# Kernel tuning notes

Measured on AMD Instinct MI355X. Metric: run time of the kernel, lower is better.

## Reference

```python
import jax, jax.numpy as jnp
import numpy as np

K = 2            # kernel_size
NQ = K * K       # 4 qubits
DEPTH = 1


def _apply1(state, U, q):
    # state: (N,2,2,2,2) complex; apply 2x2 gate U on qubit q
    s = jnp.moveaxis(state, 1 + q, -1)
    s = s @ U.T
    return jnp.moveaxis(s, -1, 1 + q)


def _cnot(state, c, t):
    s = jnp.moveaxis(state, (1 + c, 1 + t), (-2, -1))  # (...,2c,2t)
    s = jnp.stack([s[..., 0, :], s[..., 1, ::-1]], axis=-2)
    return jnp.moveaxis(s, (-2, -1), (1 + c, 1 + t))


def _rx(w):
    c, s = jnp.cos(w / 2), jnp.sin(w / 2)
    return jnp.array([[1, 0], [0, 1]], jnp.complex64) * c + jnp.array([[0, -1j], [-1j, 0]], jnp.complex64) * s


def _ry(w):
    c, s = jnp.cos(w / 2), jnp.sin(w / 2)
    return jnp.array([[1, 0], [0, 1]], jnp.complex64) * c + jnp.array([[0, -1], [1, 0]], jnp.complex64) * s


def setup_inputs() -> dict:
    key = jax.random.key(0)
    k1, k2, k3 = jax.random.split(key, 3)
    B, C, H = 1024, 1, 28
    F = H - K + 1
    n_feat = NQ * C * F * F  # 2916
    x = jax.random.uniform(k1, (B, C, H, H), dtype=jnp.float32)
    W = jax.random.normal(k2, (10, n_feat), dtype=jnp.float32)
    b = jax.random.normal(k3, (10,), dtype=jnp.float32)
    weights = jnp.zeros((DEPTH, NQ), dtype=jnp.float32)  # forward() uses zeros, not the Parameter
    return {"x": x, "W": W, "b": b, "weights": weights}


def reference(x, W, b, weights):
    B, C, H, _ = x.shape
    F = H - K + 1
    # extract all KxK patches, row-major within the patch (matches img[c,i:i+k,j:j+k].reshape(-1))
    p = jnp.stack([x[:, :, i:i + F, j:j + F] for i in range(K) for j in range(K)], axis=-1)  # (B,C,F,F,4)
    ang = p.reshape(-1, NQ) * jnp.pi  # AngleEmbedding angles, (N,4)
    # product state from per-qubit RY(theta)|0> = [cos(t/2), sin(t/2)]
    a = jnp.stack([jnp.cos(ang / 2), jnp.sin(ang / 2)], axis=-1).astype(jnp.complex64)  # (N,4,2)
    state = jnp.einsum('na,nb,nc,nd->nabcd', a[:, 0], a[:, 1], a[:, 2], a[:, 3])
    for l in range(DEPTH):
        w = weights[l]
        state = _apply1(state, _rx(w[0]), 0)
        state = _apply1(state, _rx(w[1]), 1)
        state = _cnot(state, 2, 3)
        state = _cnot(state, 0, 2)
        state = _cnot(state, 0, 3)
        state = _apply1(state, _ry(w[2]), 0)
        state = _apply1(state, _ry(w[3]), 3)
    probs = state.real ** 2 + state.imag ** 2  # (N,2,2,2,2)
    z = jnp.array([1.0, -1.0], dtype=x.dtype)
    evs = []
    for q in range(NQ):
        axes = tuple(ax for ax in range(1, 5) if ax != 1 + q)
        evs.append(probs.sum(axes) @ z)  # <Z_q>, (N,)
    evs = jnp.stack(evs, axis=-1)  # (N, 4)
    # per-image reorder: (C*F*F, 4) -> transpose -> (4*C, F, F)
    q = evs.reshape(B, C, F, F, NQ)
    q = jnp.transpose(q, (0, 4, 1, 2, 3)).reshape(B, NQ * C * F * F)
    return q @ W.T + b
```

## Files before the change

### kernel.cpp

```cpp
#include <hip/hip_runtime.h>


#define HD 28
#define NPIX 784
#define FD 27
#define NPATCH 729
#define NF 2916
#define NG 729
#define NOUT 10
#define PSTR 257
#define IM 2

__global__ __launch_bounds__(256)
void hqnn_fused(const float* __restrict__ x,
                const float* __restrict__ W,
                const float* __restrict__ bias,
                const float* __restrict__ wts,
                float* __restrict__ out)
{
    __shared__ __align__(16) float evl[IM][NF];
    __shared__ union U {
        struct { float sc[IM][NPIX]; float ss[IM][NPIX]; } tr;
        float part[IM * NOUT][PSTR];
    } u;

    const int tid = threadIdx.x;

    const float w0 = wts[0], w1 = wts[1], w2 = wts[2], w3 = wts[3];
    const float cw0 = cosf(w0);
    const float cw1 = cosf(w1);
    const float cw2 = cosf(w2), sw2 = sinf(w2);
    const float cw3 = cosf(w3), sw3 = sinf(w3);

    const float4* xb4 = (const float4*)(x + blockIdx.x * (IM * NPIX));
    for (int t = tid; t < IM * NPIX / 4; t += 256) {
        const float4 v = xb4[t];
        const int p4  = t * 4;
        const int img = (p4 >= NPIX) ? 1 : 0;
        const int off = p4 - img * NPIX;
        float s0, c0, s1, c1, s2, c2, s3, c3;
        sincospif(v.x, &s0, &c0);
        sincospif(v.y, &s1, &c1);
        sincospif(v.z, &s2, &c2);
        sincospif(v.w, &s3, &c3);
        u.tr.sc[img][off]     = c0; u.tr.ss[img][off]     = s0;
        u.tr.sc[img][off + 1] = c1; u.tr.ss[img][off + 1] = s1;
        u.tr.sc[img][off + 2] = c2; u.tr.ss[img][off + 2] = s2;
        u.tr.sc[img][off + 3] = c3; u.tr.ss[img][off + 3] = s3;
    }
    __syncthreads();

    for (int pp = tid; pp < IM * NPATCH; pp += 256) {
        const int img = pp / NPATCH;
        const int pa  = pp - img * NPATCH;
        const int fi  = pa / FD;
        const int fj  = pa - fi * FD;
        const int p   = fi * HD + fj;

        const float c00 = u.tr.sc[img][p];
        const float c01 = u.tr.sc[img][p + 1];
        const float c10 = u.tr.sc[img][p + HD];
        const float c11 = u.tr.sc[img][p + HD + 1];
        const float s00 = u.tr.ss[img][p];
        const float s10 = u.tr.ss[img][p + HD];
        const float s11 = u.tr.ss[img][p + HD + 1];

        const float ev2 = cw0 * c00 * c10;
        evl[img][pa]               = cw2 * cw0 * c00 - sw2 * s00 * s10;
        evl[img][NPATCH + pa]      = cw1 * c01;
        evl[img][2 * NPATCH + pa]  = ev2;
        evl[img][3 * NPATCH + pa]  = cw3 * ev2 * c11 - sw3 * s11;
    }
    __syncthreads();

    float acc[IM][NOUT];
#pragma unroll
    for (int m = 0; m < IM; ++m)
#pragma unroll
        for (int o = 0; o < NOUT; ++o) acc[m][o] = 0.f;

    const float4* W4 = (const float4*)W;
    const float4* e0 = (const float4*)evl[0];
    const float4* e1 = (const float4*)evl[1];
    for (int g = tid; g < NG; g += 256) {
        const float4 a = e0[g];
        const float4 c = e1[g];
#pragma unroll
        for (int o = 0; o < NOUT; ++o) {
            const float4 w = W4[o * NG + g];
            acc[0][o] += a.x * w.x + a.y * w.y + a.z * w.z + a.w * w.w;
            acc[1][o] += c.x * w.x + c.y * w.y + c.z * w.z + c.w * w.w;
        }
    }

#pragma unroll
    for (int m = 0; m < IM; ++m)
#pragma unroll
        for (int o = 0; o < NOUT; ++o) u.part[m * NOUT + o][tid] = acc[m][o];
    __syncthreads();

    if (tid < IM * NOUT * 8) {
        const int row = tid >> 3;
        const int j   = tid & 7;
        float s = 0.f;
#pragma unroll
        for (int k = 0; k < 256; k += 8) s += u.part[row][j + k];
        s += __shfl_down(s, 4, 8);
        s += __shfl_down(s, 2, 8);
        s += __shfl_down(s, 1, 8);
        if (j == 0) {
            const int img = (row >= NOUT) ? 1 : 0;
            const int o   = row - img * NOUT;
            out[(blockIdx.x * IM + img) * NOUT + o] = s + bias[o];
        }
    }
}

extern "C" void kernel_launch(void* const* d_in, const int* in_sizes, int n_in,
                              void* d_out, int out_size, void* d_ws, size_t ws_size,
                              hipStream_t stream) {
    const float* x    = (const float*)d_in[0];
    const float* W    = (const float*)d_in[1];
    const float* bias = (const float*)d_in[2];
    const float* wts  = (const float*)d_in[3];
    float* out = (float*)d_out;

    const int B = in_sizes[0] / NPIX;
    hqnn_fused<<<B / IM, 256, 0, stream>>>(x, W, bias, wts, out);
}
```

Measured before the change: 65.28 us.

## Process four images per block to halve W reloads, staging trig in two passes

Raises the number of images per block from 2 to 4, so each W float4 load from global/L2 is reused across four images. The trig staging buffers shrink to two images and are filled in two passes. The evl buffer now shares memory with the reduction partials, which needs an extra barrier. This trades fewer blocks (256 instead of 512, on a GPU with 256 CUs) and more accumulator registers for less W traffic.

```diff
diff --git a/kernel.cpp b/kernel.cpp
--- a/kernel.cpp
+++ b/kernel.cpp
@@ -9,7 +9,7 @@
 #define NG 729
 #define NOUT 10
 #define PSTR 257
-#define IM 2
+#define IM 4
 
 __global__ __launch_bounds__(256)
 void hqnn_fused(const float* __restrict__ x,
@@ -18,11 +18,12 @@
                 const float* __restrict__ wts,
                 float* __restrict__ out)
 {
-    __shared__ __align__(16) float evl[IM][NF];
-    __shared__ union U {
-        struct { float sc[IM][NPIX]; float ss[IM][NPIX]; } tr;
+    __shared__ float sc[2][NPIX];
+    __shared__ float ss[2][NPIX];
+    __shared__ __align__(16) union V {
+        float evl[IM][NF];
         float part[IM * NOUT][PSTR];
-    } u;
+    } v;
 
     const int tid = threadIdx.x;
 
@@ -33,45 +34,50 @@
     const float cw3 = cosf(w3), sw3 = sinf(w3);
 
     const float4* xb4 = (const float4*)(x + blockIdx.x * (IM * NPIX));
-    for (int t = tid; t < IM * NPIX / 4; t += 256) {
-        const float4 v = xb4[t];
-        const int p4  = t * 4;
-        const int img = (p4 >= NPIX) ? 1 : 0;
-        const int off = p4 - img * NPIX;
-        float s0, c0, s1, c1, s2, c2, s3, c3;
-        sincospif(v.x, &s0, &c0);
-        sincospif(v.y, &s1, &c1);
-        sincospif(v.z, &s2, &c2);
-        sincospif(v.w, &s3, &c3);
-        u.tr.sc[img][off]     = c0; u.tr.ss[img][off]     = s0;
-        u.tr.sc[img][off + 1] = c1; u.tr.ss[img][off + 1] = s1;
-        u.tr.sc[img][off + 2] = c2; u.tr.ss[img][off + 2] = s2;
-        u.tr.sc[img][off + 3] = c3; u.tr.ss[img][off + 3] = s3;
+
+#pragma unroll
+    for (int pass = 0; pass < 2; ++pass) {
+        for (int t = tid; t < 2 * NPIX / 4; t += 256) {
+            const float4 vpx = xb4[pass * (2 * NPIX / 4) + t];
+            const int gp   = t * 4;
+            const int imgl = (gp >= NPIX) ? 1 : 0;
+            const int off  = gp - imgl * NPIX;
+            float s0, c0, s1, c1, s2, c2, s3, c3;
+            sincospif(vpx.x, &s0, &c0);
+            sincospif(vpx.y, &s1, &c1);
+            sincospif(vpx.z, &s2, &c2);
+            sincospif(vpx.w, &s3, &c3);
+            sc[imgl][off]     = c0; ss[imgl][off]     = s0;
+            sc[imgl][off + 1] = c1; ss[imgl][off + 1] = s1;
+            sc[imgl][off + 2] = c2; ss[imgl][off + 2] = s2;
+            sc[imgl][off + 3] = c3; ss[imgl][off + 3] = s3;
+        }
+        __syncthreads();
+
+        for (int pp = tid; pp < 2 * NPATCH; pp += 256) {
+            const int imgl = pp / NPATCH;
+            const int pa   = pp - imgl * NPATCH;
+            const int fi   = pa / FD;
+            const int fj   = pa - fi * FD;
+            const int p    = fi * HD + fj;
+
+            const float c00 = sc[imgl][p];
+            const float c01 = sc[imgl][p + 1];
+            const float c10 = sc[imgl][p + HD];
+            const float c11 = sc[imgl][p + HD + 1];
+            const float s00 = ss[imgl][p];
+            const float s10 = ss[imgl][p + HD];
+            const float s11 = ss[imgl][p + HD + 1];
+
+            const int m = 2 * pass + imgl;
+            const float ev2 = cw0 * c00 * c10;
+            v.evl[m][pa]              = cw2 * cw0 * c00 - sw2 * s00 * s10;
+            v.evl[m][NPATCH + pa]     = cw1 * c01;
+            v.evl[m][2 * NPATCH + pa] = ev2;
+            v.evl[m][3 * NPATCH + pa] = cw3 * ev2 * c11 - sw3 * s11;
+        }
+        __syncthreads();
     }
-    __syncthreads();
-
-    for (int pp = tid; pp < IM * NPATCH; pp += 256) {
-        const int img = pp / NPATCH;
-        const int pa  = pp - img * NPATCH;
-        const int fi  = pa / FD;
-        const int fj  = pa - fi * FD;
-        const int p   = fi * HD + fj;
-
-        const float c00 = u.tr.sc[img][p];
-        const float c01 = u.tr.sc[img][p + 1];
-        const float c10 = u.tr.sc[img][p + HD];
-        const float c11 = u.tr.sc[img][p + HD + 1];
-        const float s00 = u.tr.ss[img][p];
-        const float s10 = u.tr.ss[img][p + HD];
-        const float s11 = u.tr.ss[img][p + HD + 1];
-
-        const float ev2 = cw0 * c00 * c10;
-        evl[img][pa]               = cw2 * cw0 * c00 - sw2 * s00 * s10;
-        evl[img][NPATCH + pa]      = cw1 * c01;
-        evl[img][2 * NPATCH + pa]  = ev2;
-        evl[img][3 * NPATCH + pa]  = cw3 * ev2 * c11 - sw3 * s11;
-    }
-    __syncthreads();
 
     float acc[IM][NOUT];
 #pragma unroll
@@ -80,36 +86,38 @@
         for (int o = 0; o < NOUT; ++o) acc[m][o] = 0.f;
 
     const float4* W4 = (const float4*)W;
-    const float4* e0 = (const float4*)evl[0];
-    const float4* e1 = (const float4*)evl[1];
     for (int g = tid; g < NG; g += 256) {
-        const float4 a = e0[g];
-        const float4 c = e1[g];
+        float4 e[IM];
+#pragma unroll
+        for (int m = 0; m < IM; ++m) e[m] = ((const float4*)v.evl[m])[g];
 #pragma unroll
         for (int o = 0; o < NOUT; ++o) {
             const float4 w = W4[o * NG + g];
-            acc[0][o] += a.x * w.x + a.y * w.y + a.z * w.z + a.w * w.w;
-            acc[1][o] += c.x * w.x + c.y * w.y + c.z * w.z + c.w * w.w;
+#pragma unroll
+            for (int m = 0; m < IM; ++m) {
+                acc[m][o] += e[m].x * w.x + e[m].y * w.y
+                           + e[m].z * w.z + e[m].w * w.w;
+            }
         }
     }
+    __syncthreads();
 
 #pragma unroll
     for (int m = 0; m < IM; ++m)
 #pragma unroll
-        for (int o = 0; o < NOUT; ++o) u.part[m * NOUT + o][tid] = acc[m][o];
+        for (int o = 0; o < NOUT; ++o) v.part[m * NOUT + o][tid] = acc[m][o];
     __syncthreads();
 
-    if (tid < IM * NOUT * 8) {
-        const int row = tid >> 3;
-        const int j   = tid & 7;
+    if (tid < IM * NOUT * 4) {
+        const int row = tid >> 2;
+        const int j   = tid & 3;
         float s = 0.f;
 #pragma unroll
-        for (int k = 0; k < 256; k += 8) s += u.part[row][j + k];
-        s += __shfl_down(s, 4, 8);
-        s += __shfl_down(s, 2, 8);
-        s += __shfl_down(s, 1, 8);
+        for (int k = 0; k < 256; k += 4) s += v.part[row][j + k];
+        s += __shfl_down(s, 2, 4);
+        s += __shfl_down(s, 1, 4);
         if (j == 0) {
-            const int img = (row >= NOUT) ? 1 : 0;
+            const int img = row / NOUT;
             const int o   = row - img * NOUT;
             out[(blockIdx.x * IM + img) * NOUT + o] = s + bias[o];
         }
```

Result: slower. 67.21 us (+2.9%).
